# Performance work log

Measured on AMD Instinct MI355X. Metric: run time of the kernel, lower is better.

Reference implementation:

```python
import jax, jax.numpy as jnp
import numpy as np

B, S, D_FF = 2, 2048, 1024
NUM_HEADS, D_KV = 16, 64
INNER = NUM_HEADS * D_KV


def setup_inputs() -> dict:
    key = jax.random.key(0)
    ks = jax.random.split(key, 8)
    scale = 1.0 / np.sqrt(D_FF)
    return {
        "q": jax.random.normal(ks[0], (B, S, D_FF), jnp.float32),
        "k": jax.random.normal(ks[1], (B, S, D_FF), jnp.float32),
        "v": jax.random.normal(ks[2], (B, S, D_FF), jnp.float32),
        "attn_mask": jax.random.normal(ks[3], (B, 1, S, S), jnp.float32),
        "Wq": jax.random.normal(ks[4], (INNER, D_FF), jnp.float32) * scale,
        "Wk": jax.random.normal(ks[5], (INNER, D_FF), jnp.float32) * scale,
        "Wv": jax.random.normal(ks[6], (INNER, D_FF), jnp.float32) * scale,
        "Wo": jax.random.normal(ks[7], (D_FF, INNER), jnp.float32) * scale,
        "num_heads": NUM_HEADS,
    }


def reference(q, k, v, attn_mask, Wq, Wk, Wv, Wo, num_heads):
    b, s, _ = q.shape
    # torch Linear (no bias): x @ W.T with W of shape [out, in]
    def proj_heads(x, W):
        y = jnp.einsum("bsd,ed->bse", x, W)  # [B,S,inner]
        return y.reshape(b, s, num_heads, -1).transpose(0, 2, 1, 3)  # [B,H,S,dk]

    qh = proj_heads(q, Wq)
    kh = proj_heads(k, Wk)
    vh = proj_heads(v, Wv)
    # T5 attention: NO 1/sqrt(d) scaling; additive mask bias before softmax
    scores = jnp.einsum("bhqd,bhkd->bhqk", qh, kh) + attn_mask  # [B,H,S,S]
    probs = jax.nn.softmax(scores, axis=-1)
    ctx = jnp.einsum("bhqk,bhkd->bhqd", probs, vh)  # [B,H,S,dk]
    ctx = ctx.transpose(0, 2, 1, 3).reshape(b, s, -1)  # [B,S,inner]
    return jnp.einsum("bse,de->bsd", ctx, Wo)  # [B,S,d_ff]
```

## Files before the change

kernel.cpp:

```cpp
#include <hip/hip_runtime.h>
#include <hip/hip_bf16.h>


typedef __attribute__((ext_vector_type(8))) short short8_t;
typedef __attribute__((ext_vector_type(4))) short short4_t;
typedef __attribute__((ext_vector_type(4))) float f32x4_t;

#define SEQ 2048
#define HEADS 16
#define DK 64
#define DFF 1024

__device__ __forceinline__ unsigned short f32_to_bf16(float f) {
  unsigned int u = __float_as_uint(f);
  u += 0x7FFFu + ((u >> 16) & 1u);
  return (unsigned short)(u >> 16);
}
__device__ __forceinline__ float bf16_to_f32(unsigned short h) {
  return __uint_as_float(((unsigned int)h) << 16);
}

__device__ __forceinline__ void gload_lds16(const void* g, void* l) {
  __builtin_amdgcn_global_load_lds(
      (__attribute__((address_space(1))) void*)(g),
      (__attribute__((address_space(3))) void*)(l), 16, 0, 0);
}

__global__ void cvt_x_kernel(const float* __restrict__ q,
                             const float* __restrict__ k,
                             const float* __restrict__ v,
                             short* __restrict__ dst, int n) {
  const float* src = (blockIdx.y == 0) ? q : (blockIdx.y == 1) ? k : v;
  short* out = dst + (size_t)blockIdx.y * n;
  int i = (blockIdx.x * 256 + threadIdx.x) * 4;
  if (i >= n) return;
  float4 f = *(const float4*)(src + i);
  short4_t s;
  s[0] = (short)f32_to_bf16(f.x);
  s[1] = (short)f32_to_bf16(f.y);
  s[2] = (short)f32_to_bf16(f.z);
  s[3] = (short)f32_to_bf16(f.w);
  *(short4_t*)(out + i) = s;
}

__global__ void cvt_w_kernel(const float* __restrict__ Wq,
                             const float* __restrict__ Wk,
                             const float* __restrict__ Wv,
                             const float* __restrict__ Wo,
                             short* __restrict__ wbase, int n) {
  int y = blockIdx.y;
  const float* src = (y == 0) ? Wq : (y == 1) ? Wk : (y == 2) ? Wv : Wo;
  int i = (blockIdx.x * 256 + threadIdx.x) * 4;
  if (i >= n) return;
  float4 f = *(const float4*)(src + i);
  float ff[4] = {f.x, f.y, f.z, f.w};
  if (y < 3) {
    short* hi = wbase + (size_t)(2 * y) * n;
    short* lo = wbase + (size_t)(2 * y + 1) * n;
    short4_t h, l;
#pragma unroll
    for (int j = 0; j < 4; ++j) {
      unsigned short hh = f32_to_bf16(ff[j]);
      h[j] = (short)hh;
      l[j] = (short)f32_to_bf16(ff[j] - bf16_to_f32(hh));
    }
    *(short4_t*)(hi + i) = h;
    *(short4_t*)(lo + i) = l;
  } else {
    short* out = wbase + (size_t)6 * n;
    short4_t s;
#pragma unroll
    for (int j = 0; j < 4; ++j) s[j] = (short)f32_to_bf16(ff[j]);
    *(short4_t*)(out + i) = s;
  }
}

template <int EPI>
__global__ __launch_bounds__(256, 2) void gemm_proj(
    const short* __restrict__ A, const short* __restrict__ Bh,
    const short* __restrict__ Bl, short* __restrict__ Ohi,
    short* __restrict__ Olo, int M, int K) {
  __shared__ short As[128 * 32];
  __shared__ short Bsh[64 * 32];
  __shared__ short Bsl[64 * 32];

  const int tid = threadIdx.x;
  const int w = tid >> 6, l = tid & 63, g = l >> 4, c = l & 15;
  const int wr = w >> 1, wc = w & 1;
  const int m0 = blockIdx.y * 128, n0 = blockIdx.x * 64;

  f32x4_t acc[4][2] = {};

  for (int k0 = 0; k0 < K; k0 += 32) {
#pragma unroll
    for (int j = 0; j < 2; ++j) {
      int e = (w * 2 + j) * 512 + l * 8;
      int r = e >> 5, cc = e & 31;
      gload_lds16(A + (size_t)(m0 + r) * K + k0 + cc, &As[(w * 2 + j) * 512]);
    }
    {
      int e = w * 512 + l * 8;
      int r = e >> 5, cc = e & 31;
      gload_lds16(Bh + (size_t)(n0 + r) * K + k0 + cc, &Bsh[w * 512]);
      gload_lds16(Bl + (size_t)(n0 + r) * K + k0 + cc, &Bsl[w * 512]);
    }
    __syncthreads();

    short8_t a[4], bh[2], bl[2];
#pragma unroll
    for (int mi = 0; mi < 4; ++mi)
      a[mi] = *(const short8_t*)(&As[(wr * 64 + mi * 16 + c) * 32 + g * 8]);
#pragma unroll
    for (int ni = 0; ni < 2; ++ni) {
      bh[ni] = *(const short8_t*)(&Bsh[(wc * 32 + ni * 16 + c) * 32 + g * 8]);
      bl[ni] = *(const short8_t*)(&Bsl[(wc * 32 + ni * 16 + c) * 32 + g * 8]);
    }
#pragma unroll
    for (int mi = 0; mi < 4; ++mi)
#pragma unroll
      for (int ni = 0; ni < 2; ++ni) {
        acc[mi][ni] = __builtin_amdgcn_mfma_f32_16x16x32_bf16(
            a[mi], bh[ni], acc[mi][ni], 0, 0, 0);
        acc[mi][ni] = __builtin_amdgcn_mfma_f32_16x16x32_bf16(
            a[mi], bl[ni], acc[mi][ni], 0, 0, 0);
      }
    __syncthreads();
  }

#pragma unroll
  for (int mi = 0; mi < 4; ++mi) {
#pragma unroll
    for (int ni = 0; ni < 2; ++ni) {
      int col = n0 + wc * 32 + ni * 16 + c;
      int hh = col >> 6, dd = col & 63;
      if (EPI == 2) {
        int row0 = m0 + wr * 64 + mi * 16 + g * 4;
        int bb = row0 >> 11, ss0 = row0 & 2047;
        short4_t s4;
#pragma unroll
        for (int j = 0; j < 4; ++j) s4[j] = (short)f32_to_bf16(acc[mi][ni][j]);
        *(short4_t*)(&Ohi[(((size_t)bb * HEADS + hh) * DK + dd) * SEQ + ss0]) = s4;
      } else {
#pragma unroll
        for (int j = 0; j < 4; ++j) {
          int row = m0 + wr * 64 + mi * 16 + g * 4 + j;
          int bb = row >> 11, ss = row & 2047;
          size_t idx = (((size_t)bb * HEADS + hh) * SEQ + ss) * DK + dd;
          float x = acc[mi][ni][j];
          unsigned short xh = f32_to_bf16(x);
          Ohi[idx] = (short)xh;
          if (EPI == 0)
            Olo[idx] = (short)f32_to_bf16(x - bf16_to_f32(xh));
        }
      }
    }
  }
}

__global__ __launch_bounds__(256, 2) void gemm_out(
    const short* __restrict__ A, const short* __restrict__ Bw,
    float* __restrict__ O, int M, int K) {
  __shared__ short As[128 * 32];
  __shared__ short Bs[64 * 32];

  const int tid = threadIdx.x;
  const int w = tid >> 6, l = tid & 63, g = l >> 4, c = l & 15;
  const int wr = w >> 1, wc = w & 1;
  const int m0 = blockIdx.y * 128, n0 = blockIdx.x * 64;

  f32x4_t acc[4][2] = {};

  for (int k0 = 0; k0 < K; k0 += 32) {
#pragma unroll
    for (int j = 0; j < 2; ++j) {
      int e = (w * 2 + j) * 512 + l * 8;
      int r = e >> 5, cc = e & 31;
      gload_lds16(A + (size_t)(m0 + r) * K + k0 + cc, &As[(w * 2 + j) * 512]);
    }
    {
      int e = w * 512 + l * 8;
      int r = e >> 5, cc = e & 31;
      gload_lds16(Bw + (size_t)(n0 + r) * K + k0 + cc, &Bs[w * 512]);
    }
    __syncthreads();

    short8_t a[4], b[2];
#pragma unroll
    for (int mi = 0; mi < 4; ++mi)
      a[mi] = *(const short8_t*)(&As[(wr * 64 + mi * 16 + c) * 32 + g * 8]);
#pragma unroll
    for (int ni = 0; ni < 2; ++ni)
      b[ni] = *(const short8_t*)(&Bs[(wc * 32 + ni * 16 + c) * 32 + g * 8]);
#pragma unroll
    for (int mi = 0; mi < 4; ++mi)
#pragma unroll
      for (int ni = 0; ni < 2; ++ni)
        acc[mi][ni] = __builtin_amdgcn_mfma_f32_16x16x32_bf16(
            a[mi], b[ni], acc[mi][ni], 0, 0, 0);
    __syncthreads();
  }

#pragma unroll
  for (int mi = 0; mi < 4; ++mi)
#pragma unroll
    for (int ni = 0; ni < 2; ++ni) {
      int col = n0 + wc * 32 + ni * 16 + c;
#pragma unroll
      for (int j = 0; j < 4; ++j) {
        int row = m0 + wr * 64 + mi * 16 + g * 4 + j;
        O[(size_t)row * DFF + col] = acc[mi][ni][j];
      }
    }
}

__global__ __launch_bounds__(256, 2) void attn_kernel(
    const short* __restrict__ qhh, const short* __restrict__ qhl,
    const short* __restrict__ khh, const short* __restrict__ vt,
    const float* __restrict__ mask, short* __restrict__ ctx) {
  const int bh = blockIdx.x;
  const int b = bh >> 4;
  const int h = bh & 15;
  const int qt = blockIdx.y;
  const int tid = threadIdx.x;
  const int w = tid >> 6, l = tid & 63, g = l >> 4, c = l & 15;

  __shared__ short Khs[64 * 72];
  __shared__ short Vts[64 * 72];
  __shared__ short Ps[4][32 * 72];
  short* psw = &Ps[w][0];

  const int qrow0 = qt * 128 + w * 32;
  const short* Qbh = qhh + ((size_t)bh * SEQ + qrow0) * DK;
  const short* Qbl = qhl + ((size_t)bh * SEQ + qrow0) * DK;
  const short* Kbh = khh + (size_t)bh * SEQ * DK;
  const short* Vb  = vt  + (size_t)bh * DK * SEQ;
  const float* M0  = mask + (size_t)b * SEQ * SEQ + (size_t)(qrow0 + c) * SEQ;

  const int srow = tid >> 2;
  const int scol = (tid & 3) * 16;
  const int sofs = srow * 72 + scol;

  short8_t qfh[2][2], qfl[2][2];
#pragma unroll
  for (int mi = 0; mi < 2; ++mi)
#pragma unroll
    for (int ks = 0; ks < 2; ++ks) {
      qfh[mi][ks] = *(const short8_t*)(Qbh + (size_t)(mi * 16 + c) * DK + ks * 32 + g * 8);
      qfl[mi][ks] = *(const short8_t*)(Qbl + (size_t)(mi * 16 + c) * DK + ks * 32 + g * 8);
    }

  short8_t rkh0 = *(const short8_t*)(Kbh + (size_t)srow * DK + scol);
  short8_t rkh1 = *(const short8_t*)(Kbh + (size_t)srow * DK + scol + 8);
  short8_t rv0  = *(const short8_t*)(Vb  + (size_t)srow * SEQ + scol);
  short8_t rv1  = *(const short8_t*)(Vb  + (size_t)srow * SEQ + scol + 8);
  float4 mpre[2][4];
#pragma unroll
  for (int mi = 0; mi < 2; ++mi)
#pragma unroll
    for (int ni = 0; ni < 4; ++ni)
      mpre[mi][ni] = *(const float4*)(M0 + (size_t)(mi * 16) * SEQ + ni * 16 + g * 4);

  f32x4_t o[4][2] = {};
  float mrun[2] = {-1e30f, -1e30f};
  float lrun[2] = {0.f, 0.f};

  for (int kv0 = 0; kv0 < SEQ; kv0 += 64) {
    __syncthreads();
    *(short8_t*)(&Khs[sofs]) = rkh0;
    *(short8_t*)(&Khs[sofs + 8]) = rkh1;
    *(short8_t*)(&Vts[sofs]) = rv0;
    *(short8_t*)(&Vts[sofs + 8]) = rv1;
    __syncthreads();

    const int kv1 = kv0 + 64;
    if (kv1 < SEQ) {
      rkh0 = *(const short8_t*)(Kbh + (size_t)(kv1 + srow) * DK + scol);
      rkh1 = *(const short8_t*)(Kbh + (size_t)(kv1 + srow) * DK + scol + 8);
      rv0  = *(const short8_t*)(Vb  + (size_t)srow * SEQ + kv1 + scol);
      rv1  = *(const short8_t*)(Vb  + (size_t)srow * SEQ + kv1 + scol + 8);
    }

    f32x4_t sa[4][2] = {};
#pragma unroll
    for (int ks = 0; ks < 2; ++ks) {
      short8_t ah[4];
#pragma unroll
      for (int ni = 0; ni < 4; ++ni)
        ah[ni] = *(const short8_t*)(&Khs[(ni * 16 + c) * 72 + ks * 32 + g * 8]);
#pragma unroll
      for (int ni = 0; ni < 4; ++ni)
#pragma unroll
        for (int mi = 0; mi < 2; ++mi) {
          sa[ni][mi] = __builtin_amdgcn_mfma_f32_16x16x32_bf16(
              ah[ni], qfh[mi][ks], sa[ni][mi], 0, 0, 0);
          sa[ni][mi] = __builtin_amdgcn_mfma_f32_16x16x32_bf16(
              ah[ni], qfl[mi][ks], sa[ni][mi], 0, 0, 0);
        }
    }

#pragma unroll
    for (int mi = 0; mi < 2; ++mi)
#pragma unroll
      for (int ni = 0; ni < 4; ++ni) {
        sa[ni][mi][0] += mpre[mi][ni].x;
        sa[ni][mi][1] += mpre[mi][ni].y;
        sa[ni][mi][2] += mpre[mi][ni].z;
        sa[ni][mi][3] += mpre[mi][ni].w;
      }
    if (kv1 < SEQ) {
#pragma unroll
      for (int mi = 0; mi < 2; ++mi)
#pragma unroll
        for (int ni = 0; ni < 4; ++ni)
          mpre[mi][ni] = *(const float4*)(M0 + (size_t)(mi * 16) * SEQ + kv1 + ni * 16 + g * 4);
    }

#pragma unroll
    for (int mi = 0; mi < 2; ++mi) {
      float t = sa[0][mi][0];
#pragma unroll
      for (int ni = 0; ni < 4; ++ni)
#pragma unroll
        for (int j = 0; j < 4; ++j) t = fmaxf(t, sa[ni][mi][j]);
      t = fmaxf(t, __shfl_xor(t, 16));
      t = fmaxf(t, __shfl_xor(t, 32));
      float mold = mrun[mi];
      float mnew = fmaxf(mold, t);
      float sc = __expf(mold - mnew);
      mrun[mi] = mnew;
#pragma unroll
      for (int di = 0; di < 4; ++di)
#pragma unroll
        for (int j = 0; j < 4; ++j) o[di][mi][j] *= sc;
      float psum = 0.f;
#pragma unroll
      for (int ni = 0; ni < 4; ++ni) {
        short4_t ph;
#pragma unroll
        for (int j = 0; j < 4; ++j) {
          float p = __expf(sa[ni][mi][j] - mnew);
          psum += p;
          ph[j] = (short)f32_to_bf16(p);
        }
        *(short4_t*)(&psw[(mi * 16 + c) * 72 + ni * 16 + g * 4]) = ph;
      }
      lrun[mi] = lrun[mi] * sc + psum;
    }

#pragma unroll
    for (int ks = 0; ks < 2; ++ks) {
      short8_t pb[2];
#pragma unroll
      for (int mi = 0; mi < 2; ++mi)
        pb[mi] = *(const short8_t*)(&psw[(mi * 16 + c) * 72 + ks * 32 + g * 8]);
#pragma unroll
      for (int di = 0; di < 4; ++di) {
        short8_t av = *(const short8_t*)(&Vts[(di * 16 + c) * 72 + ks * 32 + g * 8]);
#pragma unroll
        for (int mi = 0; mi < 2; ++mi)
          o[di][mi] = __builtin_amdgcn_mfma_f32_16x16x32_bf16(
              av, pb[mi], o[di][mi], 0, 0, 0);
      }
    }
  }

  float inv[2];
#pragma unroll
  for (int mi = 0; mi < 2; ++mi) {
    float s = lrun[mi];
    s += __shfl_xor(s, 16);
    s += __shfl_xor(s, 32);
    inv[mi] = 1.f / s;
  }
  short* Cb = ctx + ((size_t)b * SEQ + qrow0) * DFF + h * DK;
#pragma unroll
  for (int mi = 0; mi < 2; ++mi)
#pragma unroll
    for (int di = 0; di < 4; ++di) {
      short4_t s4;
#pragma unroll
      for (int j = 0; j < 4; ++j)
        s4[j] = (short)f32_to_bf16(o[di][mi][j] * inv[mi]);
      *(short4_t*)(Cb + (size_t)(mi * 16 + c) * DFF + di * 16 + g * 4) = s4;
    }
}

extern "C" void kernel_launch(void* const* d_in, const int* in_sizes, int n_in,
                              void* d_out, int out_size, void* d_ws, size_t ws_size,
                              hipStream_t stream) {
  const float* q    = (const float*)d_in[0];
  const float* k    = (const float*)d_in[1];
  const float* v    = (const float*)d_in[2];
  const float* mask = (const float*)d_in[3];
  const float* Wq   = (const float*)d_in[4];
  const float* Wk   = (const float*)d_in[5];
  const float* Wv   = (const float*)d_in[6];
  const float* Wo   = (const float*)d_in[7];
  float* out = (float*)d_out;

  const size_t NQ = 4194304;
  const size_t NW = 1048576;
  short* ws   = (short*)d_ws;
  short* qbf  = ws;
  short* kbf  = ws + NQ;
  short* vbf  = ws + 2 * NQ;
  short* qh_h = ws + 3 * NQ;
  short* qh_l = ws + 4 * NQ;
  short* wbase = ws + 5 * NQ;
  short* wq_h = wbase;
  short* wq_l = wbase + NW;
  short* wk_h = wbase + 2 * NW;
  short* wk_l = wbase + 3 * NW;
  short* wv_h = wbase + 4 * NW;
  short* wv_l = wbase + 5 * NW;
  short* wob  = wbase + 6 * NW;

  short* kh_h = qbf;
  short* vtp  = kbf;
  short* ctx  = vbf;

  cvt_x_kernel<<<dim3(4096, 3), 256, 0, stream>>>(q, k, v, ws, (int)NQ);
  cvt_w_kernel<<<dim3(1024, 4), 256, 0, stream>>>(Wq, Wk, Wv, Wo, wbase, (int)NW);

  dim3 gg(16, 32);
  gemm_proj<0><<<gg, 256, 0, stream>>>(qbf, wq_h, wq_l, qh_h, qh_l, 4096, 1024);
  gemm_proj<1><<<gg, 256, 0, stream>>>(kbf, wk_h, wk_l, kh_h, nullptr, 4096, 1024);
  gemm_proj<2><<<gg, 256, 0, stream>>>(vbf, wv_h, wv_l, vtp, nullptr, 4096, 1024);

  attn_kernel<<<dim3(32, 16), 256, 0, stream>>>(qh_h, qh_l, kh_h, vtp, mask, ctx);

  gemm_out<<<gg, 256, 0, stream>>>(ctx, wob, out, 4096, 1024);
}
```

Baseline: 211.3 us.

## Split attention block into 8 waves of 16 query rows with MFMA priority hints

The attention kernel now launches 512 threads per block, and each of the 8 waves handles 16 query rows instead of 4 waves handling 32 rows each. The K/V tile staging is respread so each thread loads one 16-byte vector per tile. Per-wave register state is halved, which aims for more resident waves to hide the latency of the mask loads and the softmax. s_setprio is also raised around the MFMA sections. The cost is less reuse of each K/V fragment read from LDS per MFMA, so LDS traffic per FLOP doubles.

```diff
diff --git a/kernel.cpp b/kernel.cpp
--- a/kernel.cpp
+++ b/kernel.cpp
@@ -213,7 +213,7 @@
     }
 }
 
-__global__ __launch_bounds__(256, 2) void attn_kernel(
+__global__ __launch_bounds__(512, 4) void attn_kernel(
     const short* __restrict__ qhh, const short* __restrict__ qhl,
     const short* __restrict__ khh, const short* __restrict__ vt,
     const float* __restrict__ mask, short* __restrict__ ctx) {
@@ -226,61 +226,52 @@
 
   __shared__ short Khs[64 * 72];
   __shared__ short Vts[64 * 72];
-  __shared__ short Ps[4][32 * 72];
+  __shared__ short Ps[8][16 * 72];
   short* psw = &Ps[w][0];
 
-  const int qrow0 = qt * 128 + w * 32;
+  const int qrow0 = qt * 128 + w * 16;
   const short* Qbh = qhh + ((size_t)bh * SEQ + qrow0) * DK;
   const short* Qbl = qhl + ((size_t)bh * SEQ + qrow0) * DK;
   const short* Kbh = khh + (size_t)bh * SEQ * DK;
   const short* Vb  = vt  + (size_t)bh * DK * SEQ;
   const float* M0  = mask + (size_t)b * SEQ * SEQ + (size_t)(qrow0 + c) * SEQ;
 
-  const int srow = tid >> 2;
-  const int scol = (tid & 3) * 16;
+  const int srow = tid >> 3;
+  const int scol = (tid & 7) * 8;
   const int sofs = srow * 72 + scol;
 
-  short8_t qfh[2][2], qfl[2][2];
-#pragma unroll
-  for (int mi = 0; mi < 2; ++mi)
-#pragma unroll
-    for (int ks = 0; ks < 2; ++ks) {
-      qfh[mi][ks] = *(const short8_t*)(Qbh + (size_t)(mi * 16 + c) * DK + ks * 32 + g * 8);
-      qfl[mi][ks] = *(const short8_t*)(Qbl + (size_t)(mi * 16 + c) * DK + ks * 32 + g * 8);
-    }
-
-  short8_t rkh0 = *(const short8_t*)(Kbh + (size_t)srow * DK + scol);
-  short8_t rkh1 = *(const short8_t*)(Kbh + (size_t)srow * DK + scol + 8);
-  short8_t rv0  = *(const short8_t*)(Vb  + (size_t)srow * SEQ + scol);
-  short8_t rv1  = *(const short8_t*)(Vb  + (size_t)srow * SEQ + scol + 8);
-  float4 mpre[2][4];
-#pragma unroll
-  for (int mi = 0; mi < 2; ++mi)
-#pragma unroll
-    for (int ni = 0; ni < 4; ++ni)
-      mpre[mi][ni] = *(const float4*)(M0 + (size_t)(mi * 16) * SEQ + ni * 16 + g * 4);
-
-  f32x4_t o[4][2] = {};
-  float mrun[2] = {-1e30f, -1e30f};
-  float lrun[2] = {0.f, 0.f};
+  short8_t qfh[2], qfl[2];
+#pragma unroll
+  for (int ks = 0; ks < 2; ++ks) {
+    qfh[ks] = *(const short8_t*)(Qbh + (size_t)c * DK + ks * 32 + g * 8);
+    qfl[ks] = *(const short8_t*)(Qbl + (size_t)c * DK + ks * 32 + g * 8);
+  }
+
+  short8_t rkh = *(const short8_t*)(Kbh + (size_t)srow * DK + scol);
+  short8_t rv  = *(const short8_t*)(Vb  + (size_t)srow * SEQ + scol);
+  float4 mpre[4];
+#pragma unroll
+  for (int ni = 0; ni < 4; ++ni)
+    mpre[ni] = *(const float4*)(M0 + ni * 16 + g * 4);
+
+  f32x4_t o[4] = {};
+  float mrun = -1e30f;
+  float lrun = 0.f;
 
   for (int kv0 = 0; kv0 < SEQ; kv0 += 64) {
     __syncthreads();
-    *(short8_t*)(&Khs[sofs]) = rkh0;
-    *(short8_t*)(&Khs[sofs + 8]) = rkh1;
-    *(short8_t*)(&Vts[sofs]) = rv0;
-    *(short8_t*)(&Vts[sofs + 8]) = rv1;
+    *(short8_t*)(&Khs[sofs]) = rkh;
+    *(short8_t*)(&Vts[sofs]) = rv;
     __syncthreads();
 
     const int kv1 = kv0 + 64;
     if (kv1 < SEQ) {
-      rkh0 = *(const short8_t*)(Kbh + (size_t)(kv1 + srow) * DK + scol);
-      rkh1 = *(const short8_t*)(Kbh + (size_t)(kv1 + srow) * DK + scol + 8);
-      rv0  = *(const short8_t*)(Vb  + (size_t)srow * SEQ + kv1 + scol);
-      rv1  = *(const short8_t*)(Vb  + (size_t)srow * SEQ + kv1 + scol + 8);
-    }
-
-    f32x4_t sa[4][2] = {};
+      rkh = *(const short8_t*)(Kbh + (size_t)(kv1 + srow) * DK + scol);
+      rv  = *(const short8_t*)(Vb  + (size_t)srow * SEQ + kv1 + scol);
+    }
+
+    f32x4_t sa[4] = {};
+    __builtin_amdgcn_s_setprio(1);
 #pragma unroll
     for (int ks = 0; ks < 2; ++ks) {
       short8_t ah[4];
@@ -288,101 +279,86 @@
       for (int ni = 0; ni < 4; ++ni)
         ah[ni] = *(const short8_t*)(&Khs[(ni * 16 + c) * 72 + ks * 32 + g * 8]);
 #pragma unroll
+      for (int ni = 0; ni < 4; ++ni) {
+        sa[ni] = __builtin_amdgcn_mfma_f32_16x16x32_bf16(
+            ah[ni], qfh[ks], sa[ni], 0, 0, 0);
+        sa[ni] = __builtin_amdgcn_mfma_f32_16x16x32_bf16(
+            ah[ni], qfl[ks], sa[ni], 0, 0, 0);
+      }
+    }
+    __builtin_amdgcn_s_setprio(0);
+
+#pragma unroll
+    for (int ni = 0; ni < 4; ++ni) {
+      sa[ni][0] += mpre[ni].x;
+      sa[ni][1] += mpre[ni].y;
+      sa[ni][2] += mpre[ni].z;
+      sa[ni][3] += mpre[ni].w;
+    }
+    if (kv1 < SEQ) {
+#pragma unroll
       for (int ni = 0; ni < 4; ++ni)
-#pragma unroll
-        for (int mi = 0; mi < 2; ++mi) {
-          sa[ni][mi] = __builtin_amdgcn_mfma_f32_16x16x32_bf16(
-              ah[ni], qfh[mi][ks], sa[ni][mi], 0, 0, 0);
-          sa[ni][mi] = __builtin_amdgcn_mfma_f32_16x16x32_bf16(
-              ah[ni], qfl[mi][ks], sa[ni][mi], 0, 0, 0);
-        }
-    }
-
-#pragma unroll
-    for (int mi = 0; mi < 2; ++mi)
-#pragma unroll
-      for (int ni = 0; ni < 4; ++ni) {
-        sa[ni][mi][0] += mpre[mi][ni].x;
-        sa[ni][mi][1] += mpre[mi][ni].y;
-        sa[ni][mi][2] += mpre[mi][ni].z;
-        sa[ni][mi][3] += mpre[mi][ni].w;
-      }
-    if (kv1 < SEQ) {
-#pragma unroll
-      for (int mi = 0; mi < 2; ++mi)
-#pragma unroll
-        for (int ni = 0; ni < 4; ++ni)
-          mpre[mi][ni] = *(const float4*)(M0 + (size_t)(mi * 16) * SEQ + kv1 + ni * 16 + g * 4);
-    }
-
-#pragma unroll
-    for (int mi = 0; mi < 2; ++mi) {
-      float t = sa[0][mi][0];
+        mpre[ni] = *(const float4*)(M0 + kv1 + ni * 16 + g * 4);
+    }
+
+    {
+      float t = sa[0][0];
 #pragma unroll
       for (int ni = 0; ni < 4; ++ni)
 #pragma unroll
-        for (int j = 0; j < 4; ++j) t = fmaxf(t, sa[ni][mi][j]);
+        for (int j = 0; j < 4; ++j) t = fmaxf(t, sa[ni][j]);
       t = fmaxf(t, __shfl_xor(t, 16));
       t = fmaxf(t, __shfl_xor(t, 32));
-      float mold = mrun[mi];
+      float mold = mrun;
       float mnew = fmaxf(mold, t);
       float sc = __expf(mold - mnew);
-      mrun[mi] = mnew;
+      mrun = mnew;
 #pragma unroll
       for (int di = 0; di < 4; ++di)
 #pragma unroll
-        for (int j = 0; j < 4; ++j) o[di][mi][j] *= sc;
+        for (int j = 0; j < 4; ++j) o[di][j] *= sc;
       float psum = 0.f;
 #pragma unroll
       for (int ni = 0; ni < 4; ++ni) {
         short4_t ph;
 #pragma unroll
         for (int j = 0; j < 4; ++j) {
-          float p = __expf(sa[ni][mi][j] - mnew);
+          float p = __expf(sa[ni][j] - mnew);
           psum += p;
           ph[j] = (short)f32_to_bf16(p);
         }
-        *(short4_t*)(&psw[(mi * 16 + c) * 72 + ni * 16 + g * 4]) = ph;
-      }
-      lrun[mi] = lrun[mi] * sc + psum;
-    }
-
+        *(short4_t*)(&psw[c * 72 + ni * 16 + g * 4]) = ph;
+      }
+      lrun = lrun * sc + psum;
+    }
+
+    __builtin_amdgcn_s_setprio(1);
 #pragma unroll
     for (int ks = 0; ks < 2; ++ks) {
-      short8_t pb[2];
-#pragma unroll
-      for (int mi = 0; mi < 2; ++mi)
-        pb[mi] = *(const short8_t*)(&psw[(mi * 16 + c) * 72 + ks * 32 + g * 8]);
+      short8_t pb = *(const short8_t*)(&psw[c * 72 + ks * 32 + g * 8]);
 #pragma unroll
       for (int di = 0; di < 4; ++di) {
         short8_t av = *(const short8_t*)(&Vts[(di * 16 + c) * 72 + ks * 32 + g * 8]);
-#pragma unroll
-        for (int mi = 0; mi < 2; ++mi)
-          o[di][mi] = __builtin_amdgcn_mfma_f32_16x16x32_bf16(
-              av, pb[mi], o[di][mi], 0, 0, 0);
-      }
-    }
-  }
-
-  float inv[2];
-#pragma unroll
-  for (int mi = 0; mi < 2; ++mi) {
-    float s = lrun[mi];
-    s += __shfl_xor(s, 16);
-    s += __shfl_xor(s, 32);
-    inv[mi] = 1.f / s;
-  }
+        o[di] = __builtin_amdgcn_mfma_f32_16x16x32_bf16(
+            av, pb, o[di], 0, 0, 0);
+      }
+    }
+    __builtin_amdgcn_s_setprio(0);
+  }
+
+  float s = lrun;
+  s += __shfl_xor(s, 16);
+  s += __shfl_xor(s, 32);
+  float inv = 1.f / s;
   short* Cb = ctx + ((size_t)b * SEQ + qrow0) * DFF + h * DK;
 #pragma unroll
-  for (int mi = 0; mi < 2; ++mi)
-#pragma unroll
-    for (int di = 0; di < 4; ++di) {
-      short4_t s4;
-#pragma unroll
-      for (int j = 0; j < 4; ++j)
-        s4[j] = (short)f32_to_bf16(o[di][mi][j] * inv[mi]);
-      *(short4_t*)(Cb + (size_t)(mi * 16 + c) * DFF + di * 16 + g * 4) = s4;
-    }
+  for (int di = 0; di < 4; ++di) {
+    short4_t s4;
+#pragma unroll
+    for (int j = 0; j < 4; ++j)
+      s4[j] = (short)f32_to_bf16(o[di][j] * inv);
+    *(short4_t*)(Cb + (size_t)c * DFF + di * 16 + g * 4) = s4;
+  }
 }
 
 extern "C" void kernel_launch(void* const* d_in, const int* in_sizes, int n_in,
@@ -427,7 +403,7 @@
   gemm_proj<1><<<gg, 256, 0, stream>>>(kbf, wk_h, wk_l, kh_h, nullptr, 4096, 1024);
   gemm_proj<2><<<gg, 256, 0, stream>>>(vbf, wv_h, wv_l, vtp, nullptr, 4096, 1024);
 
-  attn_kernel<<<dim3(32, 16), 256, 0, stream>>>(qh_h, qh_l, kh_h, vtp, mask, ctx);
+  attn_kernel<<<dim3(32, 16), 512, 0, stream>>>(qh_h, qh_l, kh_h, vtp, mask, ctx);
 
   gemm_out<<<gg, 256, 0, stream>>>(ctx, wob, out, 4096, 1024);
 }
```

After: 203.1 us. 3.9% less time.

## Split attention KV range across two wave groups with merge, exp2 softmax, lazy rescale

Applied to the files above, without the earlier changes.

Attention blocks grow to 512 threads, and two groups of four waves each process half of the KV sequence for the same query rows. Their partial outputs and running max/sum are merged through shared memory at the end. Softmax moves to base-2 (LOG2E folded into the Q projection and the mask), skips rescaling unless the row max grows by more than a threshold, uses packed bf16 conversion, and raises wave priority around the MFMA sections. The mask is now loaded directly each tile instead of being prefetched. This is meant to double parallelism per block and cut exp/rescale work, at the cost of extra shared memory, a merge step and more exposed mask load latency.

```diff
diff --git a/kernel.cpp b/kernel.cpp
--- a/kernel.cpp
+++ b/kernel.cpp
@@ -10,6 +10,7 @@
 #define HEADS 16
 #define DK 64
 #define DFF 1024
+#define LOG2E 1.44269504088896340736f
 
 __device__ __forceinline__ unsigned short f32_to_bf16(float f) {
   unsigned int u = __float_as_uint(f);
@@ -18,6 +19,11 @@
 }
 __device__ __forceinline__ float bf16_to_f32(unsigned short h) {
   return __uint_as_float(((unsigned int)h) << 16);
+}
+__device__ __forceinline__ unsigned int cvt_pk_bf16(float a, float b) {
+  unsigned int r;
+  asm("v_cvt_pk_bf16_f32 %0, %1, %2" : "=v"(r) : "v"(a), "v"(b));
+  return r;
 }
 
 __device__ __forceinline__ void gload_lds16(const void* g, void* l) {
@@ -147,6 +153,7 @@
           int bb = row >> 11, ss = row & 2047;
           size_t idx = (((size_t)bb * HEADS + hh) * SEQ + ss) * DK + dd;
           float x = acc[mi][ni][j];
+          if (EPI == 0) x *= LOG2E;
           unsigned short xh = f32_to_bf16(x);
           Ohi[idx] = (short)xh;
           if (EPI == 0)
@@ -213,7 +220,7 @@
     }
 }
 
-__global__ __launch_bounds__(256, 2) void attn_kernel(
+__global__ __launch_bounds__(512, 4) void attn_kernel(
     const short* __restrict__ qhh, const short* __restrict__ qhl,
     const short* __restrict__ khh, const short* __restrict__ vt,
     const float* __restrict__ mask, short* __restrict__ ctx) {
@@ -223,22 +230,29 @@
   const int qt = blockIdx.y;
   const int tid = threadIdx.x;
   const int w = tid >> 6, l = tid & 63, g = l >> 4, c = l & 15;
-
-  __shared__ short Khs[64 * 72];
-  __shared__ short Vts[64 * 72];
-  __shared__ short Ps[4][32 * 72];
-  short* psw = &Ps[w][0];
-
-  const int qrow0 = qt * 128 + w * 32;
+  const int grp = w >> 2;
+  const int pw = w & 3;
+  const int kvbase = grp * 1024;
+
+  __shared__ short smem[36864];
+  short* Ks = smem + grp * 9216;
+  short* Vs = smem + grp * 9216 + 4608;
+  short* psw = smem + 18432 + w * 2304;
+
+  const int qrow0 = qt * 128 + pw * 32;
   const short* Qbh = qhh + ((size_t)bh * SEQ + qrow0) * DK;
   const short* Qbl = qhl + ((size_t)bh * SEQ + qrow0) * DK;
   const short* Kbh = khh + (size_t)bh * SEQ * DK;
   const short* Vb  = vt  + (size_t)bh * DK * SEQ;
   const float* M0  = mask + (size_t)b * SEQ * SEQ + (size_t)(qrow0 + c) * SEQ;
 
-  const int srow = tid >> 2;
-  const int scol = (tid & 3) * 16;
+  const int sgrp = tid >> 8;
+  const int tl = tid & 255;
+  const int srow = tl >> 2, scol = (tl & 3) * 16;
   const int sofs = srow * 72 + scol;
+  short* sK = smem + sgrp * 9216;
+  short* sV = smem + sgrp * 9216 + 4608;
+  const int skvb = sgrp * 1024;
 
   short8_t qfh[2][2], qfl[2][2];
 #pragma unroll
@@ -249,44 +263,40 @@
       qfl[mi][ks] = *(const short8_t*)(Qbl + (size_t)(mi * 16 + c) * DK + ks * 32 + g * 8);
     }
 
-  short8_t rkh0 = *(const short8_t*)(Kbh + (size_t)srow * DK + scol);
-  short8_t rkh1 = *(const short8_t*)(Kbh + (size_t)srow * DK + scol + 8);
-  short8_t rv0  = *(const short8_t*)(Vb  + (size_t)srow * SEQ + scol);
-  short8_t rv1  = *(const short8_t*)(Vb  + (size_t)srow * SEQ + scol + 8);
-  float4 mpre[2][4];
-#pragma unroll
-  for (int mi = 0; mi < 2; ++mi)
-#pragma unroll
-    for (int ni = 0; ni < 4; ++ni)
-      mpre[mi][ni] = *(const float4*)(M0 + (size_t)(mi * 16) * SEQ + ni * 16 + g * 4);
+  short8_t rkh0 = *(const short8_t*)(Kbh + (size_t)(skvb + srow) * DK + scol);
+  short8_t rkh1 = *(const short8_t*)(Kbh + (size_t)(skvb + srow) * DK + scol + 8);
+  short8_t rv0  = *(const short8_t*)(Vb  + (size_t)srow * SEQ + skvb + scol);
+  short8_t rv1  = *(const short8_t*)(Vb  + (size_t)srow * SEQ + skvb + scol + 8);
 
   f32x4_t o[4][2] = {};
   float mrun[2] = {-1e30f, -1e30f};
   float lrun[2] = {0.f, 0.f};
 
-  for (int kv0 = 0; kv0 < SEQ; kv0 += 64) {
-    __syncthreads();
-    *(short8_t*)(&Khs[sofs]) = rkh0;
-    *(short8_t*)(&Khs[sofs + 8]) = rkh1;
-    *(short8_t*)(&Vts[sofs]) = rv0;
-    *(short8_t*)(&Vts[sofs + 8]) = rv1;
-    __syncthreads();
-
-    const int kv1 = kv0 + 64;
-    if (kv1 < SEQ) {
-      rkh0 = *(const short8_t*)(Kbh + (size_t)(kv1 + srow) * DK + scol);
-      rkh1 = *(const short8_t*)(Kbh + (size_t)(kv1 + srow) * DK + scol + 8);
-      rv0  = *(const short8_t*)(Vb  + (size_t)srow * SEQ + kv1 + scol);
-      rv1  = *(const short8_t*)(Vb  + (size_t)srow * SEQ + kv1 + scol + 8);
-    }
+  for (int t = 0; t < 16; ++t) {
+    __syncthreads();
+    *(short8_t*)(&sK[sofs]) = rkh0;
+    *(short8_t*)(&sK[sofs + 8]) = rkh1;
+    *(short8_t*)(&sV[sofs]) = rv0;
+    *(short8_t*)(&sV[sofs + 8]) = rv1;
+    __syncthreads();
+
+    if (t + 1 < 16) {
+      int kvn = skvb + (t + 1) * 64;
+      rkh0 = *(const short8_t*)(Kbh + (size_t)(kvn + srow) * DK + scol);
+      rkh1 = *(const short8_t*)(Kbh + (size_t)(kvn + srow) * DK + scol + 8);
+      rv0  = *(const short8_t*)(Vb  + (size_t)srow * SEQ + kvn + scol);
+      rv1  = *(const short8_t*)(Vb  + (size_t)srow * SEQ + kvn + scol + 8);
+    }
+    const int kvg = kvbase + t * 64;
 
     f32x4_t sa[4][2] = {};
+    __builtin_amdgcn_s_setprio(1);
 #pragma unroll
     for (int ks = 0; ks < 2; ++ks) {
       short8_t ah[4];
 #pragma unroll
       for (int ni = 0; ni < 4; ++ni)
-        ah[ni] = *(const short8_t*)(&Khs[(ni * 16 + c) * 72 + ks * 32 + g * 8]);
+        ah[ni] = *(const short8_t*)(&Ks[(ni * 16 + c) * 72 + ks * 32 + g * 8]);
 #pragma unroll
       for (int ni = 0; ni < 4; ++ni)
 #pragma unroll
@@ -297,56 +307,55 @@
               ah[ni], qfl[mi][ks], sa[ni][mi], 0, 0, 0);
         }
     }
+    __builtin_amdgcn_s_setprio(0);
 
 #pragma unroll
     for (int mi = 0; mi < 2; ++mi)
 #pragma unroll
       for (int ni = 0; ni < 4; ++ni) {
-        sa[ni][mi][0] += mpre[mi][ni].x;
-        sa[ni][mi][1] += mpre[mi][ni].y;
-        sa[ni][mi][2] += mpre[mi][ni].z;
-        sa[ni][mi][3] += mpre[mi][ni].w;
-      }
-    if (kv1 < SEQ) {
-#pragma unroll
-      for (int mi = 0; mi < 2; ++mi)
-#pragma unroll
-        for (int ni = 0; ni < 4; ++ni)
-          mpre[mi][ni] = *(const float4*)(M0 + (size_t)(mi * 16) * SEQ + kv1 + ni * 16 + g * 4);
-    }
+        float4 mv = *(const float4*)(M0 + (size_t)(mi * 16) * SEQ + kvg + ni * 16 + g * 4);
+        sa[ni][mi][0] = fmaf(mv.x, LOG2E, sa[ni][mi][0]);
+        sa[ni][mi][1] = fmaf(mv.y, LOG2E, sa[ni][mi][1]);
+        sa[ni][mi][2] = fmaf(mv.z, LOG2E, sa[ni][mi][2]);
+        sa[ni][mi][3] = fmaf(mv.w, LOG2E, sa[ni][mi][3]);
+      }
 
 #pragma unroll
     for (int mi = 0; mi < 2; ++mi) {
-      float t = sa[0][mi][0];
+      float tmx = sa[0][mi][0];
 #pragma unroll
       for (int ni = 0; ni < 4; ++ni)
 #pragma unroll
-        for (int j = 0; j < 4; ++j) t = fmaxf(t, sa[ni][mi][j]);
-      t = fmaxf(t, __shfl_xor(t, 16));
-      t = fmaxf(t, __shfl_xor(t, 32));
-      float mold = mrun[mi];
-      float mnew = fmaxf(mold, t);
-      float sc = __expf(mold - mnew);
-      mrun[mi] = mnew;
-#pragma unroll
-      for (int di = 0; di < 4; ++di)
-#pragma unroll
-        for (int j = 0; j < 4; ++j) o[di][mi][j] *= sc;
+        for (int j = 0; j < 4; ++j) tmx = fmaxf(tmx, sa[ni][mi][j]);
+      tmx = fmaxf(tmx, __shfl_xor(tmx, 16));
+      tmx = fmaxf(tmx, __shfl_xor(tmx, 32));
+      if (!__all(tmx - mrun[mi] <= 8.f)) {
+        float mnew = fmaxf(mrun[mi], tmx);
+        float sc = exp2f(mrun[mi] - mnew);
+        mrun[mi] = mnew;
+        lrun[mi] *= sc;
+#pragma unroll
+        for (int di = 0; di < 4; ++di)
+#pragma unroll
+          for (int j = 0; j < 4; ++j) o[di][mi][j] *= sc;
+      }
       float psum = 0.f;
 #pragma unroll
       for (int ni = 0; ni < 4; ++ni) {
-        short4_t ph;
-#pragma unroll
-        for (int j = 0; j < 4; ++j) {
-          float p = __expf(sa[ni][mi][j] - mnew);
-          psum += p;
-          ph[j] = (short)f32_to_bf16(p);
-        }
-        *(short4_t*)(&psw[(mi * 16 + c) * 72 + ni * 16 + g * 4]) = ph;
-      }
-      lrun[mi] = lrun[mi] * sc + psum;
-    }
-
+        float p0 = exp2f(sa[ni][mi][0] - mrun[mi]);
+        float p1 = exp2f(sa[ni][mi][1] - mrun[mi]);
+        float p2 = exp2f(sa[ni][mi][2] - mrun[mi]);
+        float p3 = exp2f(sa[ni][mi][3] - mrun[mi]);
+        psum += (p0 + p1) + (p2 + p3);
+        unsigned int u0 = cvt_pk_bf16(p0, p1);
+        unsigned int u1 = cvt_pk_bf16(p2, p3);
+        unsigned long long pu = ((unsigned long long)u1 << 32) | u0;
+        *(unsigned long long*)(&psw[(mi * 16 + c) * 72 + ni * 16 + g * 4]) = pu;
+      }
+      lrun[mi] += psum;
+    }
+
+    __builtin_amdgcn_s_setprio(1);
 #pragma unroll
     for (int ks = 0; ks < 2; ++ks) {
       short8_t pb[2];
@@ -355,34 +364,57 @@
         pb[mi] = *(const short8_t*)(&psw[(mi * 16 + c) * 72 + ks * 32 + g * 8]);
 #pragma unroll
       for (int di = 0; di < 4; ++di) {
-        short8_t av = *(const short8_t*)(&Vts[(di * 16 + c) * 72 + ks * 32 + g * 8]);
+        short8_t av = *(const short8_t*)(&Vs[(di * 16 + c) * 72 + ks * 32 + g * 8]);
 #pragma unroll
         for (int mi = 0; mi < 2; ++mi)
           o[di][mi] = __builtin_amdgcn_mfma_f32_16x16x32_bf16(
               av, pb[mi], o[di][mi], 0, 0, 0);
       }
     }
-  }
-
-  float inv[2];
-#pragma unroll
-  for (int mi = 0; mi < 2; ++mi) {
-    float s = lrun[mi];
-    s += __shfl_xor(s, 16);
-    s += __shfl_xor(s, 32);
-    inv[mi] = 1.f / s;
-  }
-  short* Cb = ctx + ((size_t)b * SEQ + qrow0) * DFF + h * DK;
-#pragma unroll
-  for (int mi = 0; mi < 2; ++mi)
-#pragma unroll
-    for (int di = 0; di < 4; ++di) {
-      short4_t s4;
-#pragma unroll
-      for (int j = 0; j < 4; ++j)
-        s4[j] = (short)f32_to_bf16(o[di][mi][j] * inv[mi]);
-      *(short4_t*)(Cb + (size_t)(mi * 16 + c) * DFF + di * 16 + g * 4) = s4;
-    }
+    __builtin_amdgcn_s_setprio(0);
+  }
+
+  __syncthreads();
+  float* R = ((float*)smem) + pw * 2304;
+  if (w >= 4) {
+#pragma unroll
+    for (int mi = 0; mi < 2; ++mi) {
+      float* Rq = R + (mi * 16 + c) * 72;
+#pragma unroll
+      for (int di = 0; di < 4; ++di)
+#pragma unroll
+        for (int j = 0; j < 4; ++j)
+          Rq[di * 16 + g * 4 + j] = o[di][mi][j];
+      Rq[65 + g] = lrun[mi];
+      if (g == 0) Rq[64] = mrun[mi];
+    }
+  }
+  __syncthreads();
+  if (w < 4) {
+    short* Cb = ctx + ((size_t)b * SEQ + qrow0) * DFF + h * DK;
+#pragma unroll
+    for (int mi = 0; mi < 2; ++mi) {
+      float* Rq = R + (mi * 16 + c) * 72;
+      float mB = Rq[64], lB = Rq[65 + g];
+      float M = fmaxf(mrun[mi], mB);
+      float sA = exp2f(mrun[mi] - M);
+      float sB = exp2f(mB - M);
+      float lm = lrun[mi] * sA + lB * sB;
+      lm += __shfl_xor(lm, 16);
+      lm += __shfl_xor(lm, 32);
+      float inv = 1.f / lm;
+#pragma unroll
+      for (int di = 0; di < 4; ++di) {
+        short4_t s4;
+#pragma unroll
+        for (int j = 0; j < 4; ++j) {
+          float val = (o[di][mi][j] * sA + Rq[di * 16 + g * 4 + j] * sB) * inv;
+          s4[j] = (short)f32_to_bf16(val);
+        }
+        *(short4_t*)(Cb + (size_t)(mi * 16 + c) * DFF + di * 16 + g * 4) = s4;
+      }
+    }
+  }
 }
 
 extern "C" void kernel_launch(void* const* d_in, const int* in_sizes, int n_in,
@@ -427,7 +459,7 @@
   gemm_proj<1><<<gg, 256, 0, stream>>>(kbf, wk_h, wk_l, kh_h, nullptr, 4096, 1024);
   gemm_proj<2><<<gg, 256, 0, stream>>>(vbf, wv_h, wv_l, vtp, nullptr, 4096, 1024);
 
-  attn_kernel<<<dim3(32, 16), 256, 0, stream>>>(qh_h, qh_l, kh_h, vtp, mask, ctx);
+  attn_kernel<<<dim3(32, 16), 512, 0, stream>>>(qh_h, qh_l, kh_h, vtp, mask, ctx);
 
   gemm_out<<<gg, 256, 0, stream>>>(ctx, wob, out, 4096, 1024);
 }
```

Result: slower. 326.6 us (+54.6%).

## Double-buffer K/V tiles, use exp2 softmax with lazy rescaling in attention

Applied to the files above, without the earlier changes.

The attention kernel now keeps two K/V tiles in shared memory and writes the next tile while the current one is consumed, so each iteration needs one barrier instead of two. The LDS row stride grows to 76 to change the bank mapping. The Q projection is pre-scaled by log2(e) and the mask is folded in with an FMA, so softmax can use exp2 directly; the running max is only updated when it rises by more than 8, which skips most rescales of the output accumulators. It also adds packed bf16 conversion and s_setprio around the MFMA blocks. In exchange it uses more shared memory, which can lower occupancy, and the lazy max lets unnormalized exponents grow up to 2^8.

```diff
diff --git a/kernel.cpp b/kernel.cpp
--- a/kernel.cpp
+++ b/kernel.cpp
@@ -10,6 +10,8 @@
 #define HEADS 16
 #define DK 64
 #define DFF 1024
+#define LOG2E 1.44269504088896340736f
+#define LSTR 76
 
 __device__ __forceinline__ unsigned short f32_to_bf16(float f) {
   unsigned int u = __float_as_uint(f);
@@ -18,6 +20,14 @@
 }
 __device__ __forceinline__ float bf16_to_f32(unsigned short h) {
   return __uint_as_float(((unsigned int)h) << 16);
+}
+__device__ __forceinline__ unsigned int cvt_pk_bf16(float a, float b) {
+  unsigned int r;
+  asm("v_cvt_pk_bf16_f32 %0, %1, %2" : "=v"(r) : "v"(a), "v"(b));
+  return r;
+}
+__device__ __forceinline__ float fexp2(float x) {
+  return __builtin_amdgcn_exp2f(x);
 }
 
 __device__ __forceinline__ void gload_lds16(const void* g, void* l) {
@@ -147,6 +157,7 @@
           int bb = row >> 11, ss = row & 2047;
           size_t idx = (((size_t)bb * HEADS + hh) * SEQ + ss) * DK + dd;
           float x = acc[mi][ni][j];
+          if (EPI == 0) x *= LOG2E;
           unsigned short xh = f32_to_bf16(x);
           Ohi[idx] = (short)xh;
           if (EPI == 0)
@@ -224,10 +235,8 @@
   const int tid = threadIdx.x;
   const int w = tid >> 6, l = tid & 63, g = l >> 4, c = l & 15;
 
-  __shared__ short Khs[64 * 72];
-  __shared__ short Vts[64 * 72];
-  __shared__ short Ps[4][32 * 72];
-  short* psw = &Ps[w][0];
+  __shared__ short smem[29184];
+  short* psw = &smem[19456 + w * 2432];
 
   const int qrow0 = qt * 128 + w * 32;
   const short* Qbh = qhh + ((size_t)bh * SEQ + qrow0) * DK;
@@ -238,7 +247,7 @@
 
   const int srow = tid >> 2;
   const int scol = (tid & 3) * 16;
-  const int sofs = srow * 72 + scol;
+  const int sofs = srow * LSTR + scol;
 
   short8_t qfh[2][2], qfl[2][2];
 #pragma unroll
@@ -249,44 +258,45 @@
       qfl[mi][ks] = *(const short8_t*)(Qbl + (size_t)(mi * 16 + c) * DK + ks * 32 + g * 8);
     }
 
-  short8_t rkh0 = *(const short8_t*)(Kbh + (size_t)srow * DK + scol);
-  short8_t rkh1 = *(const short8_t*)(Kbh + (size_t)srow * DK + scol + 8);
-  short8_t rv0  = *(const short8_t*)(Vb  + (size_t)srow * SEQ + scol);
-  short8_t rv1  = *(const short8_t*)(Vb  + (size_t)srow * SEQ + scol + 8);
+  short8_t rk0 = *(const short8_t*)(Kbh + (size_t)srow * DK + scol);
+  short8_t rk1 = *(const short8_t*)(Kbh + (size_t)srow * DK + scol + 8);
+  short8_t rv0 = *(const short8_t*)(Vb + (size_t)srow * SEQ + scol);
+  short8_t rv1 = *(const short8_t*)(Vb + (size_t)srow * SEQ + scol + 8);
+  *(short8_t*)(&smem[sofs]) = rk0;
+  *(short8_t*)(&smem[sofs + 8]) = rk1;
+  *(short8_t*)(&smem[9728 + sofs]) = rv0;
+  *(short8_t*)(&smem[9728 + sofs + 8]) = rv1;
+  rk0 = *(const short8_t*)(Kbh + (size_t)(64 + srow) * DK + scol);
+  rk1 = *(const short8_t*)(Kbh + (size_t)(64 + srow) * DK + scol + 8);
+  rv0 = *(const short8_t*)(Vb + (size_t)srow * SEQ + 64 + scol);
+  rv1 = *(const short8_t*)(Vb + (size_t)srow * SEQ + 64 + scol + 8);
+
   float4 mpre[2][4];
 #pragma unroll
   for (int mi = 0; mi < 2; ++mi)
 #pragma unroll
     for (int ni = 0; ni < 4; ++ni)
       mpre[mi][ni] = *(const float4*)(M0 + (size_t)(mi * 16) * SEQ + ni * 16 + g * 4);
+
+  __syncthreads();
 
   f32x4_t o[4][2] = {};
   float mrun[2] = {-1e30f, -1e30f};
   float lrun[2] = {0.f, 0.f};
 
-  for (int kv0 = 0; kv0 < SEQ; kv0 += 64) {
-    __syncthreads();
-    *(short8_t*)(&Khs[sofs]) = rkh0;
-    *(short8_t*)(&Khs[sofs + 8]) = rkh1;
-    *(short8_t*)(&Vts[sofs]) = rv0;
-    *(short8_t*)(&Vts[sofs + 8]) = rv1;
-    __syncthreads();
-
-    const int kv1 = kv0 + 64;
-    if (kv1 < SEQ) {
-      rkh0 = *(const short8_t*)(Kbh + (size_t)(kv1 + srow) * DK + scol);
-      rkh1 = *(const short8_t*)(Kbh + (size_t)(kv1 + srow) * DK + scol + 8);
-      rv0  = *(const short8_t*)(Vb  + (size_t)srow * SEQ + kv1 + scol);
-      rv1  = *(const short8_t*)(Vb  + (size_t)srow * SEQ + kv1 + scol + 8);
-    }
+  int cur = 0;
+  for (int t = 0; t < 32; ++t) {
+    const short* Ks = &smem[cur * 4864];
+    const short* Vs = &smem[9728 + cur * 4864];
 
     f32x4_t sa[4][2] = {};
+    __builtin_amdgcn_s_setprio(1);
 #pragma unroll
     for (int ks = 0; ks < 2; ++ks) {
       short8_t ah[4];
 #pragma unroll
       for (int ni = 0; ni < 4; ++ni)
-        ah[ni] = *(const short8_t*)(&Khs[(ni * 16 + c) * 72 + ks * 32 + g * 8]);
+        ah[ni] = *(const short8_t*)(&Ks[(ni * 16 + c) * LSTR + ks * 32 + g * 8]);
 #pragma unroll
       for (int ni = 0; ni < 4; ++ni)
 #pragma unroll
@@ -297,71 +307,96 @@
               ah[ni], qfl[mi][ks], sa[ni][mi], 0, 0, 0);
         }
     }
+    __builtin_amdgcn_s_setprio(0);
 
 #pragma unroll
     for (int mi = 0; mi < 2; ++mi)
 #pragma unroll
       for (int ni = 0; ni < 4; ++ni) {
-        sa[ni][mi][0] += mpre[mi][ni].x;
-        sa[ni][mi][1] += mpre[mi][ni].y;
-        sa[ni][mi][2] += mpre[mi][ni].z;
-        sa[ni][mi][3] += mpre[mi][ni].w;
-      }
-    if (kv1 < SEQ) {
+        sa[ni][mi][0] = fmaf(mpre[mi][ni].x, LOG2E, sa[ni][mi][0]);
+        sa[ni][mi][1] = fmaf(mpre[mi][ni].y, LOG2E, sa[ni][mi][1]);
+        sa[ni][mi][2] = fmaf(mpre[mi][ni].z, LOG2E, sa[ni][mi][2]);
+        sa[ni][mi][3] = fmaf(mpre[mi][ni].w, LOG2E, sa[ni][mi][3]);
+      }
+    if (t + 1 < 32) {
+      int kvn = (t + 1) * 64;
 #pragma unroll
       for (int mi = 0; mi < 2; ++mi)
 #pragma unroll
         for (int ni = 0; ni < 4; ++ni)
-          mpre[mi][ni] = *(const float4*)(M0 + (size_t)(mi * 16) * SEQ + kv1 + ni * 16 + g * 4);
+          mpre[mi][ni] = *(const float4*)(M0 + (size_t)(mi * 16) * SEQ + kvn + ni * 16 + g * 4);
     }
 
 #pragma unroll
     for (int mi = 0; mi < 2; ++mi) {
-      float t = sa[0][mi][0];
+      float tmx = sa[0][mi][0];
 #pragma unroll
       for (int ni = 0; ni < 4; ++ni)
 #pragma unroll
-        for (int j = 0; j < 4; ++j) t = fmaxf(t, sa[ni][mi][j]);
-      t = fmaxf(t, __shfl_xor(t, 16));
-      t = fmaxf(t, __shfl_xor(t, 32));
-      float mold = mrun[mi];
-      float mnew = fmaxf(mold, t);
-      float sc = __expf(mold - mnew);
-      mrun[mi] = mnew;
-#pragma unroll
-      for (int di = 0; di < 4; ++di)
-#pragma unroll
-        for (int j = 0; j < 4; ++j) o[di][mi][j] *= sc;
+        for (int j = 0; j < 4; ++j) tmx = fmaxf(tmx, sa[ni][mi][j]);
+      tmx = fmaxf(tmx, __shfl_xor(tmx, 16));
+      tmx = fmaxf(tmx, __shfl_xor(tmx, 32));
+      if (!__all(tmx - mrun[mi] <= 8.f)) {
+        float mnew = fmaxf(mrun[mi], tmx);
+        float sc = fexp2(mrun[mi] - mnew);
+        mrun[mi] = mnew;
+        lrun[mi] *= sc;
+#pragma unroll
+        for (int di = 0; di < 4; ++di)
+#pragma unroll
+          for (int j = 0; j < 4; ++j) o[di][mi][j] *= sc;
+      }
       float psum = 0.f;
 #pragma unroll
       for (int ni = 0; ni < 4; ++ni) {
-        short4_t ph;
-#pragma unroll
-        for (int j = 0; j < 4; ++j) {
-          float p = __expf(sa[ni][mi][j] - mnew);
-          psum += p;
-          ph[j] = (short)f32_to_bf16(p);
-        }
-        *(short4_t*)(&psw[(mi * 16 + c) * 72 + ni * 16 + g * 4]) = ph;
-      }
-      lrun[mi] = lrun[mi] * sc + psum;
-    }
-
+        float p0 = fexp2(sa[ni][mi][0] - mrun[mi]);
+        float p1 = fexp2(sa[ni][mi][1] - mrun[mi]);
+        float p2 = fexp2(sa[ni][mi][2] - mrun[mi]);
+        float p3 = fexp2(sa[ni][mi][3] - mrun[mi]);
+        psum += (p0 + p1) + (p2 + p3);
+        unsigned int u0 = cvt_pk_bf16(p0, p1);
+        unsigned int u1 = cvt_pk_bf16(p2, p3);
+        unsigned long long pu = ((unsigned long long)u1 << 32) | u0;
+        *(unsigned long long*)(&psw[(mi * 16 + c) * LSTR + ni * 16 + g * 4]) = pu;
+      }
+      lrun[mi] += psum;
+    }
+
+    __builtin_amdgcn_s_setprio(1);
 #pragma unroll
     for (int ks = 0; ks < 2; ++ks) {
       short8_t pb[2];
 #pragma unroll
       for (int mi = 0; mi < 2; ++mi)
-        pb[mi] = *(const short8_t*)(&psw[(mi * 16 + c) * 72 + ks * 32 + g * 8]);
+        pb[mi] = *(const short8_t*)(&psw[(mi * 16 + c) * LSTR + ks * 32 + g * 8]);
 #pragma unroll
       for (int di = 0; di < 4; ++di) {
-        short8_t av = *(const short8_t*)(&Vts[(di * 16 + c) * 72 + ks * 32 + g * 8]);
+        short8_t av = *(const short8_t*)(&Vs[(di * 16 + c) * LSTR + ks * 32 + g * 8]);
 #pragma unroll
         for (int mi = 0; mi < 2; ++mi)
           o[di][mi] = __builtin_amdgcn_mfma_f32_16x16x32_bf16(
               av, pb[mi], o[di][mi], 0, 0, 0);
       }
     }
+    __builtin_amdgcn_s_setprio(0);
+
+    if (t + 1 < 32) {
+      short* Kd = &smem[(cur ^ 1) * 4864];
+      short* Vd = &smem[9728 + (cur ^ 1) * 4864];
+      *(short8_t*)(&Kd[sofs]) = rk0;
+      *(short8_t*)(&Kd[sofs + 8]) = rk1;
+      *(short8_t*)(&Vd[sofs]) = rv0;
+      *(short8_t*)(&Vd[sofs + 8]) = rv1;
+      if (t + 2 < 32) {
+        int kvn = (t + 2) * 64;
+        rk0 = *(const short8_t*)(Kbh + (size_t)(kvn + srow) * DK + scol);
+        rk1 = *(const short8_t*)(Kbh + (size_t)(kvn + srow) * DK + scol + 8);
+        rv0 = *(const short8_t*)(Vb + (size_t)srow * SEQ + kvn + scol);
+        rv1 = *(const short8_t*)(Vb + (size_t)srow * SEQ + kvn + scol + 8);
+      }
+    }
+    __syncthreads();
+    cur ^= 1;
   }
 
   float inv[2];
```

Result: slower. 308.7 us (+46.1%).
